# Optimization experiments

Hardware: AMD Instinct MI355X
Metric: run time of the kernel (lower is better)

## Reference

```python
import jax, jax.numpy as jnp
import numpy as np

EPS = 1e-5

def mlp_layer(h, W, b, g, be):
    # Linear -> BatchNorm1d (training-mode batch stats over points) -> LeakyReLU
    y = h @ W + b
    mu = jnp.mean(y, axis=0)
    var = jnp.mean((y - mu) ** 2, axis=0)
    y = (y - mu) * jax.lax.rsqrt(var + EPS) * g + be
    return jax.nn.leaky_relu(y, 0.01)

def segment_unit_norm(pos, idx, S):
    # center each segment on its centroid, scale to the unit sphere, return radius*2 as diameter
    N = pos.shape[0]
    cnt = jax.ops.segment_sum(jnp.ones((N,), pos.dtype), idx, num_segments=S)
    center = jax.ops.segment_sum(pos, idx, num_segments=S) / jnp.maximum(cnt, 1.0)[:, None]
    centered = pos - center[idx]
    r2 = jax.ops.segment_max(jnp.sum(centered * centered, axis=1), idx, num_segments=S)
    r = jnp.sqrt(jnp.maximum(r2, 0.0))  # empty segments -> -inf clamped to 0
    r_safe = jnp.where(r > 0.0, r, 1.0)
    pos_n = centered / r_safe[idx][:, None]
    diameter = 2.0 * r_safe * (cnt > 0).astype(pos.dtype)
    return pos_n, diameter, cnt

def segment_max_pool(x, idx, S, cnt):
    out = jax.ops.segment_max(x, idx, num_segments=S)
    return jnp.where((cnt > 0)[:, None], out, 0.0)

def setup_inputs() -> dict:
    key = jax.random.key(0)
    ks = jax.random.split(key, 16)
    N, S = 1000000, 10000
    Cx = 64
    loc = [Cx + 3, 128, 256]
    glo = [loc[-1] + 1, 512, 512]
    d = {
        'pos': jax.random.normal(ks[0], (N, 3), jnp.float32),
        'x': jax.random.normal(ks[1], (N, Cx), jnp.float32),
        'idx': jnp.sort(jax.random.randint(ks[2], (N,), 0, S)),
        'num_segments': S,
    }
    def lin(k, fan_in, fan_out):
        s = 1.0 / np.sqrt(fan_in)
        return jax.random.uniform(k, (fan_in, fan_out), jnp.float32, -s, s)
    # local MLP params
    d['W1'], d['b1'] = lin(ks[3], loc[0], loc[1]), jnp.zeros((loc[1],), jnp.float32)
    d['g1'], d['be1'] = jnp.ones((loc[1],), jnp.float32), jnp.zeros((loc[1],), jnp.float32)
    d['W2'], d['b2'] = lin(ks[4], loc[1], loc[2]), jnp.zeros((loc[2],), jnp.float32)
    d['g2'], d['be2'] = jnp.ones((loc[2],), jnp.float32), jnp.zeros((loc[2],), jnp.float32)
    # global MLP params
    d['GW1'], d['Gb1'] = lin(ks[5], glo[0], glo[1]), jnp.zeros((glo[1],), jnp.float32)
    d['Gg1'], d['Gbe1'] = jnp.ones((glo[1],), jnp.float32), jnp.zeros((glo[1],), jnp.float32)
    d['GW2'], d['Gb2'] = lin(ks[6], glo[1], glo[2]), jnp.zeros((glo[2],), jnp.float32)
    d['Gg2'], d['Gbe2'] = jnp.ones((glo[2],), jnp.float32), jnp.zeros((glo[2],), jnp.float32)
    return d

def reference(pos, x, idx, num_segments, W1, b1, g1, be1, W2, b2, g2, be2, GW1, Gb1, Gg1, Gbe1, GW2, Gb2, Gg2, Gbe2):
    S = num_segments
    pos_n, diameter, cnt = segment_unit_norm(pos, idx, S)
    h = jnp.concatenate([x, pos_n], axis=1)            # [N, 67]
    h = mlp_layer(h, W1, b1, g1, be1)                   # [N, 128]
    h = mlp_layer(h, W2, b2, g2, be2)                   # [N, 256]
    hg = segment_max_pool(h, idx, S, cnt)               # [S, 256]
    hg = jnp.concatenate([hg, diameter[:, None]], axis=1)  # [S, 257]
    hg = mlp_layer(hg, GW1, Gb1, Gg1, Gbe1)             # [S, 512]
    hg = mlp_layer(hg, GW2, Gb2, Gg2, Gbe2)             # [S, 512]
    return hg
```

## Files before the change

### kernel.cpp

```cpp
#include <hip/hip_runtime.h>
#include <hip/hip_fp16.h>

#define LEAKY(v) ((v) < 0.0f ? 0.01f * (v) : (v))

typedef _Float16 half8 __attribute__((ext_vector_type(8)));
typedef float f32x4 __attribute__((ext_vector_type(4)));

__device__ __forceinline__ unsigned int pkrtz(float a, float b) {
  auto h = __builtin_amdgcn_cvt_pkrtz(a, b);
  union { decltype(h) h2; unsigned int u; } c; c.h2 = h; return c.u;
}
__device__ __forceinline__ unsigned short f2h(float f) {
  union { _Float16 h; unsigned short u; } c; c.h = (_Float16)f; return c.u;
}
__device__ __forceinline__ unsigned int fkey(float f) {
  unsigned int u = __float_as_uint(f);
  return ((int)u < 0) ? ~u : (u | 0x80000000u);
}
__device__ __forceinline__ float fdec(unsigned int k) {
  return __uint_as_float((k & 0x80000000u) ? (k ^ 0x80000000u) : ~k);
}


__global__ void seg_lb_kernel(const int* __restrict__ idx, int N, int S, int* __restrict__ seg_start) {
  int s = blockIdx.x * blockDim.x + threadIdx.x;
  if (s > S) return;
  int lo = 0, hi = N;
  while (lo < hi) {
    int mid = (lo + hi) >> 1;
    if (idx[mid] < s) lo = mid + 1; else hi = mid;
  }
  seg_start[s] = lo;
}

__global__ void seg_stat_kernel(const float* __restrict__ pos, const int* __restrict__ seg_start,
                                float* __restrict__ center, float* __restrict__ invr,
                                float* __restrict__ diam) {
  int s = blockIdx.x;
  int start = seg_start[s], end = seg_start[s + 1];
  int cnt = end - start;
  int lane = threadIdx.x;
  float sx = 0.f, sy = 0.f, sz = 0.f;
  for (int i = start + lane; i < end; i += 64) {
    sx += pos[3 * i + 0]; sy += pos[3 * i + 1]; sz += pos[3 * i + 2];
  }
  for (int o = 32; o > 0; o >>= 1) {
    sx += __shfl_down(sx, o); sy += __shfl_down(sy, o); sz += __shfl_down(sz, o);
  }
  float inv_cnt = 1.0f / fmaxf((float)cnt, 1.0f);
  float cx = __shfl(sx, 0) * inv_cnt;
  float cy = __shfl(sy, 0) * inv_cnt;
  float cz = __shfl(sz, 0) * inv_cnt;
  float m2 = 0.f;
  for (int i = start + lane; i < end; i += 64) {
    float dx = pos[3 * i + 0] - cx, dy = pos[3 * i + 1] - cy, dz = pos[3 * i + 2] - cz;
    m2 = fmaxf(m2, dx * dx + dy * dy + dz * dz);
  }
  for (int o = 32; o > 0; o >>= 1) m2 = fmaxf(m2, __shfl_down(m2, o));
  if (lane == 0) {
    float r = sqrtf(fmaxf(m2, 0.f));
    float rs = (r > 0.f) ? r : 1.0f;
    center[3 * s + 0] = cx; center[3 * s + 1] = cy; center[3 * s + 2] = cz;
    invr[s] = 1.0f / rs;
    diam[s] = (cnt > 0) ? 2.0f * rs : 0.0f;
  }
}


__global__ void wconv_kernel(const float* __restrict__ W, int K, int N, unsigned short* __restrict__ Wt) {
  int i = blockIdx.x * 256 + threadIdx.x;
  if (i >= N * 16) return;
  int n = i >> 4, c = i & 15;
  union { uint4 u; unsigned short h[8]; } o;
#pragma unroll
  for (int e = 0; e < 8; ++e) {
    int k = c * 8 + e;
    float v = (k < K) ? W[(size_t)k * N + n] : 0.f;
    o.h[e] = f2h(v);
  }
  *(uint4*)&Wt[(size_t)n * 128 + c * 8] = o.u;
}


__global__ __launch_bounds__(256, 2) void gemm1_kernel(
    const float* __restrict__ x, const float* __restrict__ pos, const int* __restrict__ idx,
    const float* __restrict__ center, const float* __restrict__ invr,
    const unsigned short* __restrict__ w1t, const float* __restrict__ b1,
    unsigned short* __restrict__ y1, float* __restrict__ gsum, float* __restrict__ gsq,
    int M, int ntiles) {
  __shared__ __align__(16) unsigned short Asm[128 * 128];
  __shared__ __align__(16) unsigned short Osm[128 * 128];
  const int tid = threadIdx.x;
  const int och = tid & 15;
  const int rr = tid >> 4;
  const int lane = tid & 63;
  const int wv = tid >> 6;
  const int wr = wv >> 1, wc = wv & 1;
  const int lr = lane & 15, lg = lane >> 4;
  const int tstep = gridDim.x;

  half8 b[4][3];
#pragma unroll
  for (int cf = 0; cf < 4; ++cf) {
    int n = wc * 64 + cf * 16 + lr;
#pragma unroll
    for (int ks = 0; ks < 3; ++ks) {
      int c = ks * 4 + lg;
      b[cf][ks] = *(const half8*)&w1t[n * 128 + c * 8];
    }
  }
  float bb[4];
#pragma unroll
  for (int cf = 0; cf < 4; ++cf) bb[cf] = b1[wc * 64 + cf * 16 + lr];

  if (tid < 128) {
    uint4 z = make_uint4(0u, 0u, 0u, 0u);
    int r = tid;
    *(uint4*)&Asm[r * 128 + ((9 ^ (r & 7)) << 3)] = z;
    *(uint4*)&Asm[r * 128 + ((10 ^ (r & 7)) << 3)] = z;
    *(uint4*)&Asm[r * 128 + ((11 ^ (r & 7)) << 3)] = z;
  }

  float4 pfx[8];
  float pp0 = 0.f, pp1 = 0.f, pp2 = 0.f, pc0 = 0.f, pc1 = 0.f, pc2 = 0.f, pir = 0.f;

  auto prefetch = [&](int tt) {
#pragma unroll
    for (int j = 0; j < 4; ++j) {
      int c = tid + 256 * j;
      int r = c >> 3, cc = c & 7;
      int row = tt * 128 + r;
      pfx[2 * j] = make_float4(0.f, 0.f, 0.f, 0.f);
      pfx[2 * j + 1] = make_float4(0.f, 0.f, 0.f, 0.f);
      if (row < M) {
        pfx[2 * j]     = *(const float4*)&x[(size_t)row * 64 + cc * 8];
        pfx[2 * j + 1] = *(const float4*)&x[(size_t)row * 64 + cc * 8 + 4];
      }
    }
    if (tid < 128) {
      int row = tt * 128 + tid;
      pp0 = pp1 = pp2 = pc0 = pc1 = pc2 = 0.f; pir = 0.f;
      if (row < M) {
        int s = idx[row];
        pp0 = pos[3 * row + 0]; pp1 = pos[3 * row + 1]; pp2 = pos[3 * row + 2];
        pc0 = center[3 * s + 0]; pc1 = center[3 * s + 1]; pc2 = center[3 * s + 2];
        pir = invr[s];
      }
    }
  };
  auto stageA = [&]() {
#pragma unroll
    for (int j = 0; j < 4; ++j) {
      int c = tid + 256 * j;
      int r = c >> 3, cc = c & 7;
      uint4 o;
      o.x = pkrtz(pfx[2 * j].x, pfx[2 * j].y);
      o.y = pkrtz(pfx[2 * j].z, pfx[2 * j].w);
      o.z = pkrtz(pfx[2 * j + 1].x, pfx[2 * j + 1].y);
      o.w = pkrtz(pfx[2 * j + 1].z, pfx[2 * j + 1].w);
      *(uint4*)&Asm[r * 128 + ((cc ^ (r & 7)) << 3)] = o;
    }
    if (tid < 128) {
      int r = tid;
      uint4 o = make_uint4(0u, 0u, 0u, 0u);
      o.x = pkrtz((pp0 - pc0) * pir, (pp1 - pc1) * pir);
      o.y = pkrtz((pp2 - pc2) * pir, 0.f);
      *(uint4*)&Asm[r * 128 + ((8 ^ (r & 7)) << 3)] = o;
    }
  };

  int t = blockIdx.x;
  prefetch(t);
  stageA();
  __syncthreads();

  float psum[8], psq[8];
#pragma unroll
  for (int c = 0; c < 8; ++c) { psum[c] = 0.f; psq[c] = 0.f; }

  const f32x4 fzero = {0.f, 0.f, 0.f, 0.f};

  for (;;) {
    const int tn = t + tstep;
    const bool more = tn < ntiles;
    if (more) prefetch(tn);
    f32x4 acc[4][4];
#pragma unroll
    for (int rf = 0; rf < 4; ++rf)
#pragma unroll
      for (int cf = 0; cf < 4; ++cf) acc[rf][cf] = fzero;
#pragma unroll
    for (int ks = 0; ks < 3; ++ks) {
      half8 a[4];
      int c = ks * 4 + lg;
#pragma unroll
      for (int rf = 0; rf < 4; ++rf) {
        int row = wr * 64 + rf * 16 + lr;
        a[rf] = *(const half8*)&Asm[row * 128 + ((c ^ (row & 7)) << 3)];
      }
#pragma unroll
      for (int cf = 0; cf < 4; ++cf)
#pragma unroll
        for (int rf = 0; rf < 4; ++rf)
          acc[rf][cf] = __builtin_amdgcn_mfma_f32_16x16x32_f16(a[rf], b[cf][ks], acc[rf][cf], 0, 0, 0);
    }
#pragma unroll
    for (int cf = 0; cf < 4; ++cf) {
      int col = wc * 64 + cf * 16 + lr;
#pragma unroll
      for (int rf = 0; rf < 4; ++rf) {
#pragma unroll
        for (int r = 0; r < 4; ++r) {
          int row = wr * 64 + rf * 16 + lg * 4 + r;
          Osm[row * 128 + (((col >> 3) ^ (row & 7)) << 3) + (col & 7)] = f2h(acc[rf][cf][r] + bb[cf]);
        }
      }
    }
    __syncthreads();
    const int row0 = t * 128;
#pragma unroll
    for (int j = 0; j < 8; ++j) {
      int r = rr + 16 * j;
      int row = row0 + r;
      if (row < M) {
        uint4 v = *(const uint4*)&Osm[r * 128 + ((och ^ (r & 7)) << 3)];
        *(uint4*)&y1[(size_t)row * 128 + och * 8] = v;
        union { uint4 u; _Float16 h[8]; } w; w.u = v;
#pragma unroll
        for (int c = 0; c < 8; ++c) { float f = (float)w.h[c]; psum[c] += f; psq[c] += f * f; }
      }
    }
    if (!more) break;
    stageA();
    t = tn;
    __syncthreads();
  }

  __syncthreads();
  float* redS = (float*)Osm;
  float* redQ = redS + 16 * 128;
#pragma unroll
  for (int c = 0; c < 8; ++c) {
    redS[rr * 128 + och * 8 + c] = psum[c];
    redQ[rr * 128 + och * 8 + c] = psq[c];
  }
  __syncthreads();
  if (tid < 128) {
    float s = 0.f, q = 0.f;
#pragma unroll
    for (int g = 0; g < 16; ++g) { s += redS[g * 128 + tid]; q += redQ[g * 128 + tid]; }
    atomicAdd(&gsum[tid], s);
    atomicAdd(&gsq[tid], q);
  }
}


__global__ __launch_bounds__(256, 2) void gemm2_kernel(
    const unsigned short* __restrict__ y1,
    const unsigned short* __restrict__ a1h, const unsigned short* __restrict__ c1h,
    const unsigned short* __restrict__ w2t, const float* __restrict__ b2,
    const int* __restrict__ idx,
    unsigned int* __restrict__ segmx, unsigned int* __restrict__ segmn,
    float* __restrict__ gsum, float* __restrict__ gsq,
    int M, int ntiles) {
  __shared__ __align__(16) unsigned short Abuf[2][128 * 128];
  __shared__ int sbuf[2][128];
  const int tid = threadIdx.x;
  const int col0 = blockIdx.x * 128;
  const int och = tid & 15;
  const int rr = tid >> 4;
  const int tstep = gridDim.y;

  const _Float16* ap = (const _Float16*)a1h;
  const _Float16* cp = (const _Float16*)c1h;
  _Float16 av[8], cv[8];
#pragma unroll
  for (int q = 0; q < 8; ++q) { av[q] = ap[och * 8 + q]; cv[q] = cp[och * 8 + q]; }

  int t = blockIdx.y;
  uint4 pf[8];
  auto perm = [](int p) { return (p & 0x43) | ((p & 0x30) >> 2) | ((p & 0x0c) << 2); };
#pragma unroll
  for (int j = 0; j < 8; ++j) {
    int r = rr + 16 * j;
    int row = t * 128 + perm(r);
    pf[j] = make_uint4(0u, 0u, 0u, 0u);
    if (row < M) pf[j] = *(const uint4*)&y1[(size_t)row * 128 + och * 8];
  }
  if (tid < 128) {
    int row = t * 128 + tid;
    sbuf[0][tid] = (row < M) ? idx[row] : -1;
  }

#pragma unroll
  for (int j = 0; j < 8; ++j) {
    int n = rr + 16 * j;
    uint4 v = *(const uint4*)&w2t[(size_t)(col0 + n) * 128 + och * 8];
    *(uint4*)&Abuf[0][n * 128 + ((och ^ (n & 7)) << 3)] = v;
  }
  __syncthreads();

  const int lane = tid & 63;
  const int wv = tid >> 6;
  const int wr = wv >> 1, wc = wv & 1;
  const int lr = lane & 15, lg = lane >> 4;

  half8 b[4][4];
#pragma unroll
  for (int cf = 0; cf < 4; ++cf) {
    int n = wc * 64 + cf * 16 + lr;
#pragma unroll
    for (int ks = 0; ks < 4; ++ks) {
      int c = ks * 4 + lg;
      b[cf][ks] = *(const half8*)&Abuf[0][n * 128 + ((c ^ (n & 7)) << 3)];
    }
  }
  float bb[4];
#pragma unroll
  for (int cf = 0; cf < 4; ++cf) bb[cf] = b2[col0 + wc * 64 + cf * 16 + lr];
  __syncthreads();

#pragma unroll
  for (int j = 0; j < 8; ++j) {
    int r = rr + 16 * j;
    union { uint4 u; _Float16 h[8]; } w; w.u = pf[j];
#pragma unroll
    for (int q = 0; q < 8; ++q) {
      _Float16 v = w.h[q] * av[q] + cv[q];
      w.h[q] = (v < (_Float16)0.f) ? v * (_Float16)0.01f : v;
    }
    *(uint4*)&Abuf[0][r * 128 + ((och ^ (r & 7)) << 3)] = w.u;
  }
  __syncthreads();

  float csum[4], csq[4];
#pragma unroll
  for (int cf = 0; cf < 4; ++cf) { csum[cf] = 0.f; csq[cf] = 0.f; }

  const f32x4 fzero = {0.f, 0.f, 0.f, 0.f};
  int p = 0;

  for (;;) {
    const int tn = t + tstep;
    const bool more = tn < ntiles;
    if (more) {
#pragma unroll
      for (int j = 0; j < 8; ++j) {
        int r = rr + 16 * j;
        int row = tn * 128 + perm(r);
        pf[j] = make_uint4(0u, 0u, 0u, 0u);
        if (row < M) pf[j] = *(const uint4*)&y1[(size_t)row * 128 + och * 8];
      }
      if (tid < 128) {
        int row = tn * 128 + tid;
        sbuf[p ^ 1][tid] = (row < M) ? idx[row] : -1;
      }
    }
    f32x4 acc[4][4];
#pragma unroll
    for (int rf = 0; rf < 4; ++rf)
#pragma unroll
      for (int cf = 0; cf < 4; ++cf) acc[rf][cf] = fzero;
    const unsigned short* Ac = Abuf[p];
#pragma unroll
    for (int ks = 0; ks < 4; ++ks) {
      half8 a[4];
      int c = ks * 4 + lg;
#pragma unroll
      for (int rf = 0; rf < 4; ++rf) {
        int row = wr * 64 + rf * 16 + lr;
        a[rf] = *(const half8*)&Ac[row * 128 + ((c ^ (row & 7)) << 3)];
      }
#pragma unroll
      for (int cf = 0; cf < 4; ++cf)
#pragma unroll
        for (int rf = 0; rf < 4; ++rf)
          acc[rf][cf] = __builtin_amdgcn_mfma_f32_16x16x32_f16(a[rf], b[cf][ks], acc[rf][cf], 0, 0, 0);
    }
    {
      const int* sp = &sbuf[p][wr * 64 + lg * 16];
      int4 s0 = *(const int4*)&sp[0];
      int4 s1 = *(const int4*)&sp[4];
      int4 s2 = *(const int4*)&sp[8];
      int4 s3 = *(const int4*)&sp[12];
      int sid[16] = { s0.x, s0.y, s0.z, s0.w, s1.x, s1.y, s1.z, s1.w,
                      s2.x, s2.y, s2.z, s2.w, s3.x, s3.y, s3.z, s3.w };
#pragma unroll
      for (int cf = 0; cf < 4; ++cf) {
        const unsigned col = col0 + wc * 64 + cf * 16 + lr;
        float vv[16];
#pragma unroll
        for (int rf = 0; rf < 4; ++rf)
#pragma unroll
          for (int r = 0; r < 4; ++r) vv[rf * 4 + r] = acc[rf][cf][r] + bb[cf];
#pragma unroll
        for (int k = 0; k < 16; ++k) {
          float vk = (sid[k] >= 0) ? vv[k] : 0.f;
          csum[cf] += vk; csq[cf] += vk * vk;
        }
        int cur = sid[0];
        float mx = vv[0], mn = vv[0];
#pragma unroll
        for (int k = 1; k < 16; ++k) {
          if (sid[k] != cur) {
            if (cur >= 0) {
              atomicMax(&segmx[(size_t)cur * 256 + col], fkey(mx));
              atomicMin(&segmn[(size_t)cur * 256 + col], fkey(mn));
            }
            cur = sid[k]; mx = vv[k]; mn = vv[k];
          } else {
            mx = fmaxf(mx, vv[k]); mn = fminf(mn, vv[k]);
          }
        }
        if (cur >= 0) {
          atomicMax(&segmx[(size_t)cur * 256 + col], fkey(mx));
          atomicMin(&segmn[(size_t)cur * 256 + col], fkey(mn));
        }
      }
    }
    if (!more) break;
#pragma unroll
    for (int j = 0; j < 8; ++j) {
      int r = rr + 16 * j;
      union { uint4 u; _Float16 h[8]; } w; w.u = pf[j];
#pragma unroll
      for (int q = 0; q < 8; ++q) {
        _Float16 v = w.h[q] * av[q] + cv[q];
        w.h[q] = (v < (_Float16)0.f) ? v * (_Float16)0.01f : v;
      }
      *(uint4*)&Abuf[p ^ 1][r * 128 + ((och ^ (r & 7)) << 3)] = w.u;
    }
    t = tn; p ^= 1;
    __syncthreads();
  }

#pragma unroll
  for (int cf = 0; cf < 4; ++cf) {
    csum[cf] += __shfl_xor(csum[cf], 16);
    csum[cf] += __shfl_xor(csum[cf], 32);
    csq[cf] += __shfl_xor(csq[cf], 16);
    csq[cf] += __shfl_xor(csq[cf], 32);
  }
  if (lg == 0) {
#pragma unroll
    for (int cf = 0; cf < 4; ++cf) {
      int col = col0 + wc * 64 + cf * 16 + lr;
      atomicAdd(&gsum[col], csum[cf]);
      atomicAdd(&gsq[col], csq[cf]);
    }
  }
}


__device__ __forceinline__ void mm_tile(const float* __restrict__ As, const float* __restrict__ Bs,
                                        int bk, int tr, int tc, float acc[4][8]) {
  for (int k4 = 0; k4 < bk; k4 += 4) {
    float4 a[4];
#pragma unroll
    for (int r = 0; r < 4; ++r) a[r] = *(const float4*)&As[(tr * 4 + r) * 68 + k4];
#pragma unroll
    for (int kk = 0; kk < 4; ++kk) {
      float4 w0 = *(const float4*)&Bs[(k4 + kk) * 128 + tc * 8];
      float4 w1 = *(const float4*)&Bs[(k4 + kk) * 128 + tc * 8 + 4];
#pragma unroll
      for (int r = 0; r < 4; ++r) {
        float av = (kk == 0) ? a[r].x : (kk == 1) ? a[r].y : (kk == 2) ? a[r].z : a[r].w;
        acc[r][0] = fmaf(av, w0.x, acc[r][0]);
        acc[r][1] = fmaf(av, w0.y, acc[r][1]);
        acc[r][2] = fmaf(av, w0.z, acc[r][2]);
        acc[r][3] = fmaf(av, w0.w, acc[r][3]);
        acc[r][4] = fmaf(av, w1.x, acc[r][4]);
        acc[r][5] = fmaf(av, w1.y, acc[r][5]);
        acc[r][6] = fmaf(av, w1.z, acc[r][6]);
        acc[r][7] = fmaf(av, w1.w, acc[r][7]);
      }
    }
  }
}

__device__ __forceinline__ void stats_reduce(float* redS, float* redQ,
                                             const float psum[8], const float psq[8],
                                             int tr, int tc, int tid,
                                             float* __restrict__ gsum, float* __restrict__ gsq, int col0) {
  __syncthreads();
#pragma unroll
  for (int c = 0; c < 8; ++c) {
    redS[tr * 128 + tc * 8 + c] = psum[c];
    redQ[tr * 128 + tc * 8 + c] = psq[c];
  }
  __syncthreads();
  if (tid < 128) {
    float s = 0.f, q = 0.f;
#pragma unroll
    for (int r = 0; r < 16; ++r) { s += redS[r * 128 + tid]; q += redQ[r * 128 + tid]; }
    atomicAdd(&gsum[col0 + tid], s);
    atomicAdd(&gsq[col0 + tid], q);
  }
}


template <bool NORM>
__global__ __launch_bounds__(256) void gemmG_kernel(
    const float* __restrict__ A, int lda, int K, int M,
    const float* __restrict__ an, const float* __restrict__ cn,
    const float* __restrict__ W, const float* __restrict__ bias,
    float* __restrict__ Y, float* __restrict__ gsum, float* __restrict__ gsq) {
  __shared__ float As[64 * 68];
  __shared__ float Bs[64 * 128];
  const int tid = threadIdx.x;
  const int row0 = blockIdx.x * 64;
  const int col0 = blockIdx.y * 128;
  const int tr = tid >> 4, tc = tid & 15;
  float acc[4][8];
#pragma unroll
  for (int r = 0; r < 4; ++r)
#pragma unroll
    for (int c = 0; c < 8; ++c) acc[r][c] = 0.f;

  const int nkb = (K + 63) >> 6;
  for (int kb = 0; kb < nkb; ++kb) {
    if (kb) __syncthreads();
    for (int e = tid; e < 64 * 64; e += 256) {
      int r = e >> 6, c = e & 63;
      int row = row0 + r, k = kb * 64 + c;
      float v = 0.f;
      if (row < M && k < K) {
        v = A[(size_t)row * lda + k];
        if (NORM) { v = an[k] * v + cn[k]; v = LEAKY(v); }
      }
      As[r * 68 + c] = v;
    }
    for (int e = tid; e < 64 * 32; e += 256) {
      int r = e >> 5, c4 = e & 31;
      int k = kb * 64 + r;
      float4 v = make_float4(0.f, 0.f, 0.f, 0.f);
      if (k < K) v = *(const float4*)&W[(size_t)k * 512 + col0 + c4 * 4];
      *(float4*)&Bs[r * 128 + c4 * 4] = v;
    }
    __syncthreads();
    mm_tile(As, Bs, 64, tr, tc, acc);
  }

  float psum[8], psq[8];
#pragma unroll
  for (int c = 0; c < 8; ++c) { psum[c] = 0.f; psq[c] = 0.f; }
#pragma unroll
  for (int r = 0; r < 4; ++r) {
    int row = row0 + tr * 4 + r;
    if (row < M) {
      float yv[8];
#pragma unroll
      for (int c = 0; c < 8; ++c) {
        yv[c] = acc[r][c] + bias[col0 + tc * 8 + c];
        psum[c] += yv[c]; psq[c] += yv[c] * yv[c];
      }
      *(float4*)&Y[(size_t)row * 512 + col0 + tc * 8] = make_float4(yv[0], yv[1], yv[2], yv[3]);
      *(float4*)&Y[(size_t)row * 512 + col0 + tc * 8 + 4] = make_float4(yv[4], yv[5], yv[6], yv[7]);
    }
  }
  stats_reduce(As, Bs, psum, psq, tr, tc, tid, gsum, gsq, col0);
}


__global__ void finalize_kernel(const float* __restrict__ gsum, const float* __restrict__ gsq,
                                const float* __restrict__ g, const float* __restrict__ be,
                                float invn, int C, float* __restrict__ a, float* __restrict__ c,
                                unsigned short* __restrict__ ah, unsigned short* __restrict__ chh) {
  int j = blockIdx.x * blockDim.x + threadIdx.x;
  if (j >= C) return;
  float mu = gsum[j] * invn;
  float var = gsq[j] * invn - mu * mu;
  float aj = g[j] * rsqrtf(var + 1e-5f);
  float cj = be[j] - mu * aj;
  a[j] = aj;
  c[j] = cj;
  if (ah) { ah[j] = f2h(aj); chh[j] = f2h(cj); }
}


__global__ void poolfin_kernel(const unsigned int* __restrict__ segmx, const unsigned int* __restrict__ segmn,
                               const int* __restrict__ seg_start,
                               const float* __restrict__ a2, const float* __restrict__ c2,
                               const float* __restrict__ diam, float* __restrict__ hg) {
  int s = blockIdx.x;
  int j = threadIdx.x;
  bool nonempty = seg_start[s + 1] > seg_start[s];
  float aj = a2[j], cj = c2[j];
  unsigned int k = (aj >= 0.f) ? segmx[(size_t)s * 256 + j] : segmn[(size_t)s * 256 + j];
  float f = fdec(k);
  float v = aj * f + cj;
  v = LEAKY(v);
  hg[(size_t)s * 257 + j] = nonempty ? v : 0.0f;
  if (j == 0) hg[(size_t)s * 257 + 256] = diam[s];
}


__global__ void final_kernel(const float* __restrict__ y4, const float* __restrict__ a4,
                             const float* __restrict__ c4, float* __restrict__ out, int total) {
  int i = blockIdx.x * blockDim.x + threadIdx.x;
  if (i >= total) return;
  int j = i & 511;
  float v = a4[j] * y4[i] + c4[j];
  out[i] = LEAKY(v);
}


extern "C" void kernel_launch(void* const* d_in, const int* in_sizes, int n_in,
                              void* d_out, int out_size, void* d_ws, size_t ws_size,
                              hipStream_t stream) {
  const float* pos  = (const float*)d_in[0];
  const float* x    = (const float*)d_in[1];
  const int*   idx  = (const int*)d_in[2];
  const float* W1   = (const float*)d_in[4];
  const float* b1   = (const float*)d_in[5];
  const float* g1   = (const float*)d_in[6];
  const float* be1  = (const float*)d_in[7];
  const float* W2   = (const float*)d_in[8];
  const float* b2   = (const float*)d_in[9];
  const float* g2   = (const float*)d_in[10];
  const float* be2  = (const float*)d_in[11];
  const float* GW1  = (const float*)d_in[12];
  const float* Gb1  = (const float*)d_in[13];
  const float* Gg1  = (const float*)d_in[14];
  const float* Gbe1 = (const float*)d_in[15];
  const float* GW2  = (const float*)d_in[16];
  const float* Gb2  = (const float*)d_in[17];
  const float* Gg2  = (const float*)d_in[18];
  const float* Gbe2 = (const float*)d_in[19];
  float* out = (float*)d_out;

  const int N = in_sizes[0] / 3;
  const int S = 10000;

  char* ws = (char*)d_ws;
  size_t off = 0;
  auto take = [&](size_t bytes) -> char* {
    char* p = ws + off;
    off = (off + bytes + 255) & ~(size_t)255;
    return p;
  };
  int*   seg_start = (int*)take((size_t)(S + 1) * sizeof(int));
  float* center    = (float*)take((size_t)S * 3 * sizeof(float));
  float* invr      = (float*)take((size_t)S * sizeof(float));
  float* diam      = (float*)take((size_t)S * sizeof(float));
  float* stats     = (float*)take(2816 * sizeof(float));
  float* gsum1 = stats,        *gsq1 = stats + 128;
  float* gsum2 = stats + 256,  *gsq2 = stats + 512;
  float* gsum3 = stats + 768,  *gsq3 = stats + 1280;
  float* gsum4 = stats + 1792, *gsq4 = stats + 2304;
  float* par = (float*)take(2816 * sizeof(float));
  float* a1 = par,        *c1 = par + 256;
  float* a2 = par + 512,  *c2 = par + 768;
  float* a3 = par + 1024, *c3 = par + 1536;
  float* a4 = par + 2048, *c4 = par + 2560;
  unsigned short* a1h = (unsigned short*)take(128 * 2);
  unsigned short* c1h = (unsigned short*)take(128 * 2);
  unsigned short* w1t = (unsigned short*)take((size_t)128 * 128 * 2);
  unsigned short* w2t = (unsigned short*)take((size_t)256 * 128 * 2);
  float* hg = (float*)take((size_t)S * 257 * sizeof(float));
  float* y3 = (float*)take((size_t)S * 512 * sizeof(float));
  float* y4 = (float*)take((size_t)S * 512 * sizeof(float));
  unsigned int* segmx = (unsigned int*)take((size_t)S * 256 * sizeof(unsigned int));
  unsigned int* segmn = (unsigned int*)take((size_t)S * 256 * sizeof(unsigned int));
  unsigned short* y1 = (unsigned short*)take((size_t)N * 128 * 2);
  (void)ws_size; (void)n_in; (void)out_size;

  hipMemsetAsync(stats, 0, 2816 * sizeof(float), stream);
  hipMemsetAsync(segmx, 0x00, (size_t)S * 256 * sizeof(unsigned int), stream);
  hipMemsetAsync(segmn, 0xFF, (size_t)S * 256 * sizeof(unsigned int), stream);

  wconv_kernel<<<(128 * 16 + 255) / 256, 256, 0, stream>>>(W1, 67, 128, w1t);
  wconv_kernel<<<(256 * 16 + 255) / 256, 256, 0, stream>>>(W2, 128, 256, w2t);

  seg_lb_kernel<<<(S + 1 + 255) / 256, 256, 0, stream>>>(idx, N, S, seg_start);
  seg_stat_kernel<<<S, 64, 0, stream>>>(pos, seg_start, center, invr, diam);

  const int ntiles = (N + 127) / 128;
  gemm1_kernel<<<512, 256, 0, stream>>>(x, pos, idx, center, invr, w1t, b1, y1, gsum1, gsq1, N, ntiles);
  finalize_kernel<<<1, 128, 0, stream>>>(gsum1, gsq1, g1, be1, 1.0f / (float)N, 128, a1, c1, a1h, c1h);

  gemm2_kernel<<<dim3(2, 256), 256, 0, stream>>>(y1, a1h, c1h, w2t, b2, idx, segmx, segmn,
                                                 gsum2, gsq2, N, ntiles);
  finalize_kernel<<<1, 256, 0, stream>>>(gsum2, gsq2, g2, be2, 1.0f / (float)N, 256, a2, c2, nullptr, nullptr);

  poolfin_kernel<<<S, 256, 0, stream>>>(segmx, segmn, seg_start, a2, c2, diam, hg);

  gemmG_kernel<false><<<dim3((S + 63) / 64, 4), 256, 0, stream>>>(hg, 257, 257, S, nullptr, nullptr,
                                                                  GW1, Gb1, y3, gsum3, gsq3);
  finalize_kernel<<<2, 256, 0, stream>>>(gsum3, gsq3, Gg1, Gbe1, 1.0f / (float)S, 512, a3, c3, nullptr, nullptr);

  gemmG_kernel<true><<<dim3((S + 63) / 64, 4), 256, 0, stream>>>(y3, 512, 512, S, a3, c3,
                                                                 GW2, Gb2, y4, gsum4, gsq4);
  finalize_kernel<<<2, 256, 0, stream>>>(gsum4, gsq4, Gg2, Gbe2, 1.0f / (float)S, 512, a4, c4, nullptr, nullptr);

  final_kernel<<<(S * 512 + 255) / 256, 256, 0, stream>>>(y4, a4, c4, out, S * 512);
}
```

Baseline: 690.2 us.

## Use contiguous tile chunks per block and fast-path uniform-segment pooling

Both point GEMM kernels now give each block a contiguous range of row tiles instead of striding by the grid size. Consecutive tiles then share segments within a block, which should reduce atomic contention and improve locality on the sorted segment index. gemm2 swaps its grid dimensions so the tile-chunk index is blockIdx.x and the column half is blockIdx.y. A new fast path handles a 16-row group that lies entirely in one segment: it does a straight max/min/sum reduction and issues one atomic pair per column, skipping the per-row segment-change scan. Contiguous chunks may leave the load less balanced near the end, and the added branch may cause divergence.

```diff
diff --git a/kernel.cpp b/kernel.cpp
--- a/kernel.cpp
+++ b/kernel.cpp
@@ -97,7 +97,11 @@
   const int wv = tid >> 6;
   const int wr = wv >> 1, wc = wv & 1;
   const int lr = lane & 15, lg = lane >> 4;
-  const int tstep = gridDim.x;
+
+  const int cpb = (ntiles + (int)gridDim.x - 1) / (int)gridDim.x;
+  int t = blockIdx.x * cpb;
+  const int tend = min(t + cpb, ntiles);
+  if (t >= tend) return;
 
   half8 b[4][3];
 #pragma unroll
@@ -169,7 +173,6 @@
     }
   };
 
-  int t = blockIdx.x;
   prefetch(t);
   stageA();
   __syncthreads();
@@ -181,8 +184,8 @@
   const f32x4 fzero = {0.f, 0.f, 0.f, 0.f};
 
   for (;;) {
-    const int tn = t + tstep;
-    const bool more = tn < ntiles;
+    const int tn = t + 1;
+    const bool more = tn < tend;
     if (more) prefetch(tn);
     f32x4 acc[4][4];
 #pragma unroll
@@ -266,10 +269,14 @@
   __shared__ __align__(16) unsigned short Abuf[2][128 * 128];
   __shared__ int sbuf[2][128];
   const int tid = threadIdx.x;
-  const int col0 = blockIdx.x * 128;
+  const int col0 = blockIdx.y * 128;
   const int och = tid & 15;
   const int rr = tid >> 4;
-  const int tstep = gridDim.y;
+
+  const int cpb = (ntiles + (int)gridDim.x - 1) / (int)gridDim.x;
+  int t = blockIdx.x * cpb;
+  const int tend = min(t + cpb, ntiles);
+  if (t >= tend) return;
 
   const _Float16* ap = (const _Float16*)a1h;
   const _Float16* cp = (const _Float16*)c1h;
@@ -277,7 +284,6 @@
 #pragma unroll
   for (int q = 0; q < 8; ++q) { av[q] = ap[och * 8 + q]; cv[q] = cp[och * 8 + q]; }
 
-  int t = blockIdx.y;
   uint4 pf[8];
   auto perm = [](int p) { return (p & 0x43) | ((p & 0x30) >> 2) | ((p & 0x0c) << 2); };
 #pragma unroll
@@ -341,8 +347,8 @@
   int p = 0;
 
   for (;;) {
-    const int tn = t + tstep;
-    const bool more = tn < ntiles;
+    const int tn = t + 1;
+    const bool more = tn < tend;
     if (more) {
 #pragma unroll
       for (int j = 0; j < 8; ++j) {
@@ -385,36 +391,59 @@
       int4 s3 = *(const int4*)&sp[12];
       int sid[16] = { s0.x, s0.y, s0.z, s0.w, s1.x, s1.y, s1.z, s1.w,
                       s2.x, s2.y, s2.z, s2.w, s3.x, s3.y, s3.z, s3.w };
-#pragma unroll
-      for (int cf = 0; cf < 4; ++cf) {
-        const unsigned col = col0 + wc * 64 + cf * 16 + lr;
-        float vv[16];
-#pragma unroll
-        for (int rf = 0; rf < 4; ++rf)
-#pragma unroll
-          for (int r = 0; r < 4; ++r) vv[rf * 4 + r] = acc[rf][cf][r] + bb[cf];
-#pragma unroll
-        for (int k = 0; k < 16; ++k) {
-          float vk = (sid[k] >= 0) ? vv[k] : 0.f;
-          csum[cf] += vk; csq[cf] += vk * vk;
-        }
-        int cur = sid[0];
-        float mx = vv[0], mn = vv[0];
-#pragma unroll
-        for (int k = 1; k < 16; ++k) {
-          if (sid[k] != cur) {
-            if (cur >= 0) {
-              atomicMax(&segmx[(size_t)cur * 256 + col], fkey(mx));
-              atomicMin(&segmn[(size_t)cur * 256 + col], fkey(mn));
-            }
-            cur = sid[k]; mx = vv[k]; mn = vv[k];
-          } else {
-            mx = fmaxf(mx, vv[k]); mn = fminf(mn, vv[k]);
+      bool uni = true;
+#pragma unroll
+      for (int k = 1; k < 16; ++k) uni = uni && (sid[k] == sid[0]);
+      if (uni) {
+        if (sid[0] >= 0) {
+#pragma unroll
+          for (int cf = 0; cf < 4; ++cf) {
+            const unsigned col = col0 + wc * 64 + cf * 16 + lr;
+            float mx = -3.4e38f, mn = 3.4e38f;
+#pragma unroll
+            for (int rf = 0; rf < 4; ++rf)
+#pragma unroll
+              for (int r = 0; r < 4; ++r) {
+                float v = acc[rf][cf][r] + bb[cf];
+                mx = fmaxf(mx, v); mn = fminf(mn, v);
+                csum[cf] += v; csq[cf] += v * v;
+              }
+            atomicMax(&segmx[(size_t)sid[0] * 256 + col], fkey(mx));
+            atomicMin(&segmn[(size_t)sid[0] * 256 + col], fkey(mn));
           }
         }
-        if (cur >= 0) {
-          atomicMax(&segmx[(size_t)cur * 256 + col], fkey(mx));
-          atomicMin(&segmn[(size_t)cur * 256 + col], fkey(mn));
+      } else {
+#pragma unroll
+        for (int cf = 0; cf < 4; ++cf) {
+          const unsigned col = col0 + wc * 64 + cf * 16 + lr;
+          float vv[16];
+#pragma unroll
+          for (int rf = 0; rf < 4; ++rf)
+#pragma unroll
+            for (int r = 0; r < 4; ++r) vv[rf * 4 + r] = acc[rf][cf][r] + bb[cf];
+#pragma unroll
+          for (int k = 0; k < 16; ++k) {
+            float vk = (sid[k] >= 0) ? vv[k] : 0.f;
+            csum[cf] += vk; csq[cf] += vk * vk;
+          }
+          int cur = sid[0];
+          float mx = vv[0], mn = vv[0];
+#pragma unroll
+          for (int k = 1; k < 16; ++k) {
+            if (sid[k] != cur) {
+              if (cur >= 0) {
+                atomicMax(&segmx[(size_t)cur * 256 + col], fkey(mx));
+                atomicMin(&segmn[(size_t)cur * 256 + col], fkey(mn));
+              }
+              cur = sid[k]; mx = vv[k]; mn = vv[k];
+            } else {
+              mx = fmaxf(mx, vv[k]); mn = fminf(mn, vv[k]);
+            }
+          }
+          if (cur >= 0) {
+            atomicMax(&segmx[(size_t)cur * 256 + col], fkey(mx));
+            atomicMin(&segmn[(size_t)cur * 256 + col], fkey(mn));
+          }
         }
       }
     }
@@ -679,7 +708,7 @@
   gemm1_kernel<<<512, 256, 0, stream>>>(x, pos, idx, center, invr, w1t, b1, y1, gsum1, gsq1, N, ntiles);
   finalize_kernel<<<1, 128, 0, stream>>>(gsum1, gsq1, g1, be1, 1.0f / (float)N, 128, a1, c1, a1h, c1h);
 
-  gemm2_kernel<<<dim3(2, 256), 256, 0, stream>>>(y1, a1h, c1h, w2t, b2, idx, segmx, segmn,
+  gemm2_kernel<<<dim3(256, 2), 256, 0, stream>>>(y1, a1h, c1h, w2t, b2, idx, segmx, segmn,
                                                  gsum2, gsq2, N, ntiles);
   finalize_kernel<<<1, 256, 0, stream>>>(gsum2, gsq2, g2, be2, 1.0f / (float)N, 256, a2, c2, nullptr, nullptr);
 
```

New measurement: 809.6 us. +17.3%, slower.
